# Optimization experiments

Measured on AMD Instinct MI355X. Metric: run time of the kernel, lower is better.

## Reference

```python
import jax, jax.numpy as jnp
import numpy as np

EPS = 1e-6
N_HEAD = 16

def alibi_slopes(n_head):
    # standard ALiBi geometric slopes for power-of-2 head counts
    start = 2.0 ** (-8.0 / n_head)
    return (start ** np.arange(1, n_head + 1)).astype(np.float32)

def rsig(x):
    # rational sigmoid sigma(x) = 0.5 * (x / (|x| + 1) + 1)
    return 0.5 * (x / (jnp.abs(x) + 1.0) + 1.0)

def mr_norm(x, w):
    # RationalMR: x / (mean(|x|) + eps) * weight
    return x / (jnp.mean(jnp.abs(x), axis=-1, keepdims=True) + EPS) * w


def setup_inputs() -> dict:
    key = jax.random.key(0)
    ks = jax.random.split(key, 6)
    d_model, d_ffn = 1024, 4096
    B, T = 1, 2048
    x = jax.random.normal(ks[0], (B, T, d_model), dtype=jnp.float32)
    s = 0.02
    w_qkv = jax.random.normal(ks[1], (3 * d_model, d_model), dtype=jnp.float32) * s
    w_out = jax.random.normal(ks[2], (d_model, d_model), dtype=jnp.float32) * s
    w_merged = jax.random.normal(ks[3], (2 * d_ffn, d_model), dtype=jnp.float32) * s
    w3 = jax.random.normal(ks[4], (d_model, d_ffn), dtype=jnp.float32) * s
    norm1_w = jnp.ones((d_model,), dtype=jnp.float32)
    norm2_w = jnp.ones((d_model,), dtype=jnp.float32)
    return {"x": x, "w_qkv": w_qkv, "w_out": w_out, "w_merged": w_merged,
            "w3": w3, "norm1_w": norm1_w, "norm2_w": norm2_w}


def reference(x, w_qkv, w_out, w_merged, w3, norm1_w, norm2_w):
    B, T, C = x.shape
    H = N_HEAD
    D = C // H
    scale = 1.0 / jnp.sqrt(jnp.float32(D))

    # --- attention sub-block ---
    h = mr_norm(x, norm1_w)
    qkv = (h @ w_qkv.T).reshape(B, T, 3, H, D).transpose(2, 0, 3, 1, 4)  # [3,B,H,T,D]
    q, k, v = qkv[0], qkv[1], qkv[2]
    scores = jnp.einsum('bhtd,bhsd->bhts', q, k) * scale  # [B,H,T,T]
    pos = jnp.arange(T)
    rel = jnp.abs(pos[:, None] - pos[None, :]).astype(jnp.float32)
    slopes = jnp.asarray(alibi_slopes(H))
    scores = scores - rel[None, None] * slopes[None, :, None, None]
    causal = pos[None, :] > pos[:, None]  # mask j > i
    scores = jnp.where(causal[None, None], jnp.float32(-10000.0), scores)
    # rational softmax: sigma(s)^4 / (sum sigma(s)^4 + eps)
    p4 = rsig(scores) ** 4
    probs = p4 / (jnp.sum(p4, axis=-1, keepdims=True) + EPS)
    attn = jnp.einsum('bhts,bhsd->bhtd', probs, v)  # [B,H,T,D]
    attn = attn.transpose(0, 2, 1, 3).reshape(B, T, C)
    x = x + attn @ w_out.T

    # --- FFN sub-block (rational SwiGLU) ---
    h2 = mr_norm(x, norm2_w)
    merged = h2 @ w_merged.T
    gate, val = jnp.split(merged, 2, axis=-1)
    hidden = gate * rsig(gate) * val
    x = x + hidden @ w3.T
    return x
```

## Files before the change

kernel.cpp:

```cpp
#include <hip/hip_runtime.h>
#include <hip/hip_bf16.h>
#include <stdint.h>

typedef unsigned int u32;
typedef unsigned short u16;
typedef __attribute__((ext_vector_type(8))) short bf16x8;
typedef __attribute__((ext_vector_type(4))) float f32x4;

#define MFMA(a, b, c) __builtin_amdgcn_mfma_f32_16x16x32_bf16(a, b, c, 0, 0, 0)

__device__ __forceinline__ u16 f2bf(float f) {
  u32 u = __float_as_uint(f);
  return (u16)((u + 0x7FFFu + ((u >> 16) & 1u)) >> 16);
}
__device__ __forceinline__ float bf2f(u16 h) {
  return __uint_as_float(((u32)h) << 16);
}
__device__ __forceinline__ float rsig_fast(float sc) {
  return 0.5f + 0.5f * sc * __builtin_amdgcn_rcpf(fabsf(sc) + 1.f);
}
__device__ __forceinline__ void async16(void* lds, const void* g) {
  __builtin_amdgcn_global_load_lds((const __attribute__((address_space(1))) u32*)g,
                                   (__attribute__((address_space(3))) u32*)lds, 16, 0, 0);
}

__global__ __launch_bounds__(256) void to_bf16(const float* __restrict__ src,
                                               u16* __restrict__ dst) {
  const size_t i = (size_t)blockIdx.x * 256 + threadIdx.x;
  const float4 a = ((const float4*)src)[2 * i];
  const float4 b = ((const float4*)src)[2 * i + 1];
  ushort4 o0, o1;
  o0.x = f2bf(a.x); o0.y = f2bf(a.y); o0.z = f2bf(a.z); o0.w = f2bf(a.w);
  o1.x = f2bf(b.x); o1.y = f2bf(b.y); o1.z = f2bf(b.z); o1.w = f2bf(b.w);
  ((ushort4*)dst)[2 * i] = o0;
  ((ushort4*)dst)[2 * i + 1] = o1;
}

__global__ __launch_bounds__(256) void mrnorm(const float* __restrict__ x,
                                              const float* __restrict__ wg,
                                              u16* __restrict__ out) {
  const int row = blockIdx.x;
  const int tid = threadIdx.x;
  const float4 v = ((const float4*)(x + (size_t)row * 1024))[tid];
  float s = fabsf(v.x) + fabsf(v.y) + fabsf(v.z) + fabsf(v.w);
#pragma unroll
  for (int off = 1; off < 64; off <<= 1) s += __shfl_xor(s, off);
  __shared__ float red[4];
  if ((tid & 63) == 0) red[tid >> 6] = s;
  __syncthreads();
  const float inv = 1.f / ((red[0] + red[1] + red[2] + red[3]) * (1.f / 1024.f) + 1e-6f);
  const float4 g = ((const float4*)wg)[tid];
  ushort4 o;
  o.x = f2bf(v.x * inv * g.x);
  o.y = f2bf(v.y * inv * g.y);
  o.z = f2bf(v.z * inv * g.z);
  o.w = f2bf(v.w * inv * g.w);
  ((ushort4*)out)[(size_t)row * 256 + tid] = o;
}

template <int EPI, bool DBUF>
__global__ __launch_bounds__(256) void gemm_bt(const u16* __restrict__ A, int lda,
                                               const u16* __restrict__ B, int ldb,
                                               void* __restrict__ C,
                                               const float* __restrict__ resid,
                                               int M, int N, int K) {
  __shared__ __align__(16) u16 As[(DBUF ? 2 : 1) * 128 * 64];
  __shared__ __align__(16) u16 Bs[(DBUF ? 2 : 1) * 128 * 64];
  const int tid = threadIdx.x;
  const int lane = tid & 63;
  const int w = tid >> 6;
  const int wr = (w >> 1) << 6;
  const int wc = (w & 1) << 6;
  const int nbn = N >> 7;
  const int m0 = (blockIdx.x / nbn) << 7;
  const int n0 = (blockIdx.x % nbn) << 7;
  const int l15 = lane & 15;
  const int lhi = lane >> 4;
  A += (size_t)blockIdx.y * K;
  B += (size_t)blockIdx.y * K;

  f32x4 acc[4][4] = {};

  auto stage = [&](int buf, int k0) {
#pragma unroll
    for (int p = 0; p < 4; ++p) {
      const int c = p * 256 + tid;
      const int row = c >> 3;
      const int cb = (c & 7) << 4;
      const int src = cb ^ ((row & 7) << 4);
      async16((char*)As + buf * 16384 + c * 16,
              (const char*)A + ((size_t)(m0 + row) * lda + k0) * 2 + src);
      async16((char*)Bs + buf * 16384 + c * 16,
              (const char*)B + ((size_t)(n0 + row) * ldb + k0) * 2 + src);
    }
  };
  auto compute = [&](int buf) {
#pragma unroll
    for (int kk = 0; kk < 2; ++kk) {
      bf16x8 af[4], bfr[4];
#pragma unroll
      for (int m = 0; m < 4; ++m) {
        const int row = wr + (m << 4) + l15;
        const int off = row * 128 + (((kk << 6) + (lhi << 4)) ^ ((row & 7) << 4));
        af[m] = *(const bf16x8*)((const char*)As + buf * 16384 + off);
      }
#pragma unroll
      for (int n = 0; n < 4; ++n) {
        const int row = wc + (n << 4) + l15;
        const int off = row * 128 + (((kk << 6) + (lhi << 4)) ^ ((row & 7) << 4));
        bfr[n] = *(const bf16x8*)((const char*)Bs + buf * 16384 + off);
      }
#pragma unroll
      for (int m = 0; m < 4; ++m)
#pragma unroll
        for (int n = 0; n < 4; ++n)
          acc[m][n] = MFMA(af[m], bfr[n], acc[m][n]);
    }
  };

  if (DBUF) {
    stage(0, 0);
    __syncthreads();
    int cur = 0;
    for (int k0 = 0; k0 < K; k0 += 64) {
      if (k0 + 64 < K) stage(cur ^ 1, k0 + 64);
      compute(cur);
      __syncthreads();
      cur ^= 1;
    }
  } else {
    for (int k0 = 0; k0 < K; k0 += 64) {
      stage(0, k0);
      __syncthreads();
      compute(0);
      __syncthreads();
    }
  }

  u16* Cp = (u16*)C + (size_t)blockIdx.y * M * N;
#pragma unroll
  for (int m = 0; m < 4; ++m) {
#pragma unroll
    for (int n = 0; n < 4; ++n) {
      const int col = n0 + wc + (n << 4) + l15;
#pragma unroll
      for (int r = 0; r < 4; ++r) {
        const int row = m0 + wr + (m << 4) + (lhi << 2) + r;
        const float v = acc[m][n][r];
        if (EPI == 0) {
          Cp[(size_t)row * N + col] = f2bf(v);
        } else {
          const size_t idx = (size_t)row * N + col;
          ((float*)C)[idx] = resid[idx] + v;
        }
      }
    }
  }
}

__global__ __launch_bounds__(256) void gemm_ffn1(const u16* __restrict__ A,
                                                 const u16* __restrict__ B,
                                                 u16* __restrict__ hid) {
  __shared__ __align__(16) u16 As[2][128 * 64];
  __shared__ __align__(16) u16 Bg[2][64 * 64];
  __shared__ __align__(16) u16 Bv[2][64 * 64];
  const int tid = threadIdx.x;
  const int lane = tid & 63;
  const int w = tid >> 6;
  const int wr = (w >> 1) << 6;
  const int wc = (w & 1) << 5;
  const int m0 = (blockIdx.x >> 6) << 7;
  const int n0 = (blockIdx.x & 63) << 6;
  const int l15 = lane & 15;
  const int lhi = lane >> 4;

  f32x4 ag[4][2] = {};
  f32x4 av[4][2] = {};

  auto stage = [&](int buf, int k0) {
#pragma unroll
    for (int p = 0; p < 4; ++p) {
      const int c = p * 256 + tid;
      const int row = c >> 3;
      const int cb = (c & 7) << 4;
      const int src = cb ^ ((row & 7) << 4);
      async16((char*)As[buf] + c * 16,
              (const char*)A + ((size_t)(m0 + row) * 1024 + k0) * 2 + src);
    }
#pragma unroll
    for (int p = 0; p < 2; ++p) {
      const int c = p * 256 + tid;
      const int row = c >> 3;
      const int cb = (c & 7) << 4;
      const int src = cb ^ ((row & 7) << 4);
      async16((char*)Bg[buf] + c * 16,
              (const char*)B + ((size_t)(n0 + row) * 1024 + k0) * 2 + src);
      async16((char*)Bv[buf] + c * 16,
              (const char*)B + ((size_t)(4096 + n0 + row) * 1024 + k0) * 2 + src);
    }
  };
  auto compute = [&](int buf) {
#pragma unroll
    for (int kk = 0; kk < 2; ++kk) {
      bf16x8 af[4], bgf[2], bvf[2];
#pragma unroll
      for (int m = 0; m < 4; ++m) {
        const int row = wr + (m << 4) + l15;
        const int off = row * 128 + (((kk << 6) + (lhi << 4)) ^ ((row & 7) << 4));
        af[m] = *(const bf16x8*)((const char*)As[buf] + off);
      }
#pragma unroll
      for (int n = 0; n < 2; ++n) {
        const int row = wc + (n << 4) + l15;
        const int off = row * 128 + (((kk << 6) + (lhi << 4)) ^ ((row & 7) << 4));
        bgf[n] = *(const bf16x8*)((const char*)Bg[buf] + off);
        bvf[n] = *(const bf16x8*)((const char*)Bv[buf] + off);
      }
#pragma unroll
      for (int m = 0; m < 4; ++m)
#pragma unroll
        for (int n = 0; n < 2; ++n) {
          ag[m][n] = MFMA(af[m], bgf[n], ag[m][n]);
          av[m][n] = MFMA(af[m], bvf[n], av[m][n]);
        }
    }
  };

  stage(0, 0);
  __syncthreads();
  int cur = 0;
  for (int k0 = 0; k0 < 1024; k0 += 64) {
    if (k0 + 64 < 1024) stage(cur ^ 1, k0 + 64);
    compute(cur);
    __syncthreads();
    cur ^= 1;
  }

#pragma unroll
  for (int m = 0; m < 4; ++m) {
#pragma unroll
    for (int n = 0; n < 2; ++n) {
      const int col = n0 + wc + (n << 4) + l15;
#pragma unroll
      for (int r = 0; r < 4; ++r) {
        const int row = m0 + wr + (m << 4) + (lhi << 2) + r;
        const float g = ag[m][n][r];
        const float v = av[m][n][r];
        hid[(size_t)row * 4096 + col] = f2bf(g * rsig_fast(g) * v);
      }
    }
  }
}

__global__ __launch_bounds__(256) void splitk_reduce(const u16* __restrict__ part,
                                                     const float* __restrict__ resid,
                                                     float* __restrict__ out) {
  const size_t i = ((size_t)blockIdx.x * 256 + threadIdx.x) * 8;
  const float4 r0 = *(const float4*)(resid + i);
  const float4 r1 = *(const float4*)(resid + i + 4);
  float acc[8] = {r0.x, r0.y, r0.z, r0.w, r1.x, r1.y, r1.z, r1.w};
#pragma unroll
  for (int c = 0; c < 4; ++c) {
    const uint4 p = *(const uint4*)(part + (size_t)c * 2097152 + i);
    const u16* ps = (const u16*)&p;
#pragma unroll
    for (int j = 0; j < 8; ++j) acc[j] += bf2f(ps[j]);
  }
  float4 o0 = {acc[0], acc[1], acc[2], acc[3]};
  float4 o1 = {acc[4], acc[5], acc[6], acc[7]};
  *(float4*)(out + i) = o0;
  *(float4*)(out + i + 4) = o1;
}

__global__ __launch_bounds__(256) void transpose_v(const u16* __restrict__ qkv,
                                                   u16* __restrict__ vt) {
  __shared__ __align__(16) u16 tile[64][72];
  const int head = blockIdx.x >> 5;
  const int t0 = (blockIdx.x & 31) << 6;
  const int tid = threadIdx.x;
  const int row = tid >> 2;
  const int cb = (tid & 3) << 4;
  const u16* src = qkv + (size_t)(t0 + row) * 3072 + 2048 + head * 64 + cb;
  *(uint4*)&tile[row][cb] = *(const uint4*)src;
  *(uint4*)&tile[row][cb + 8] = *(const uint4*)(src + 8);
  __syncthreads();
  u16 buf[16];
#pragma unroll
  for (int j = 0; j < 16; ++j) buf[j] = tile[cb + j][row];
  u16* dst = vt + (size_t)(head * 64 + row) * 2048 + t0 + cb;
  *(uint4*)dst = *(const uint4*)&buf[0];
  *(uint4*)(dst + 8) = *(const uint4*)&buf[8];
}

__global__ __launch_bounds__(256) void attn_part(const u16* __restrict__ qkv,
                                                 const u16* __restrict__ vt,
                                                 u16* __restrict__ pnum,
                                                 float* __restrict__ pden) {
  const int id = blockIdx.x;
  const int head = id & 15;
  const int rem = id >> 4;
  int a, g;
  if (rem < 32)      { a = 3; g = rem; }
  else if (rem < 56) { a = 2; g = rem - 32; }
  else if (rem < 72) { a = 1; g = rem - 56; }
  else               { a = 0; g = rem - 72; }
  const int qb = (a << 3) + g / (a + 1);
  const int c = g - (g / (a + 1)) * (a + 1);
  const int slot = head * 80 + ((a * (a + 1)) << 2) + (qb - (a << 3)) * (a + 1) + c;

  __shared__ __align__(16) u16 Ks[2][64 * 64];
  __shared__ __align__(16) u16 Vs[2][64 * 64];
  __shared__ __align__(16) u16 QP[4][16 * 64];
  const int tid = threadIdx.x;
  const int lane = tid & 63;
  const int w = tid >> 6;
  const int l15 = lane & 15;
  const int lhi = lane >> 4;
  const int qbase = qb << 6;
  const float slope = exp2f(-0.5f * (float)(head + 1));

  auto stageKV = [&](int buf, int s0) {
#pragma unroll
    for (int p = 0; p < 2; ++p) {
      const int cc = p * 256 + tid;
      const int row = cc >> 3;
      const int cb = (cc & 7) << 4;
      const int src = cb ^ ((row & 7) << 4);
      async16((char*)Ks[buf] + cc * 16,
              (const char*)qkv + ((size_t)(s0 + row) * 3072 + 1024 + head * 64) * 2 + src);
      async16((char*)Vs[buf] + cc * 16,
              (const char*)vt + ((size_t)(head * 64 + row) * 2048 + s0) * 2 + src);
    }
  };

  const int sfirst = c << 9;
  const int smax = min(qbase, sfirst + 448);
#pragma unroll
  for (int p = 0; p < 2; ++p) {
    const int cc = p * 256 + tid;
    const int row = cc >> 3;
    const int cb = (cc & 7) << 4;
    const int src = cb ^ ((row & 7) << 4);
    async16((char*)QP + cc * 16,
            (const char*)qkv + ((size_t)(qbase + row) * 3072 + head * 64) * 2 + src);
  }
  stageKV(0, sfirst);
  __syncthreads();

  bf16x8 qf[2];
#pragma unroll
  for (int kk = 0; kk < 2; ++kk) {
    const int row = (w << 4) + l15;
    const int off = row * 128 + (((kk << 6) + (lhi << 4)) ^ ((row & 7) << 4));
    qf[kk] = *(const bf16x8*)((const char*)QP + off);
  }

  f32x4 oacc[4] = {};
  float rs[4] = {0.f, 0.f, 0.f, 0.f};
  u16* pw = (u16*)QP[w];
  int cur = 0;

  for (int s0 = sfirst; s0 <= smax; s0 += 64) {
    if (s0 + 64 <= smax) stageKV(cur ^ 1, s0 + 64);
    const char* Kc = (const char*)Ks[cur];
    const char* Vc = (const char*)Vs[cur];

    bf16x8 kf[4][2];
#pragma unroll
    for (int bb = 0; bb < 4; ++bb)
#pragma unroll
      for (int kk = 0; kk < 2; ++kk) {
        const int row = (bb << 4) + l15;
        const int off = row * 128 + (((kk << 6) + (lhi << 4)) ^ ((row & 7) << 4));
        kf[bb][kk] = *(const bf16x8*)(Kc + off);
      }
    f32x4 sa[4];
#pragma unroll
    for (int bb = 0; bb < 4; ++bb) {
      f32x4 z = {0.f, 0.f, 0.f, 0.f};
      z = MFMA(qf[0], kf[bb][0], z);
      sa[bb] = MFMA(qf[1], kf[bb][1], z);
    }
#pragma unroll
    for (int bb = 0; bb < 4; ++bb) {
      const int s_abs = s0 + (bb << 4) + l15;
#pragma unroll
      for (int r = 0; r < 4; ++r) {
        const int prow = (lhi << 2) + r;
        const int q_abs = qbase + (w << 4) + prow;
        float p4 = 0.f;
        if (s_abs <= q_abs) {
          const float sc = sa[bb][r] * 0.125f - slope * (float)(q_abs - s_abs);
          const float t = rsig_fast(sc);
          const float t2 = t * t;
          p4 = t2 * t2;
        }
        rs[r] += p4;
        const int pcol2 = ((bb << 4) + l15) << 1;
        const int poff = prow * 128 + (pcol2 ^ ((prow & 7) << 4));
        *(u16*)((char*)pw + poff) = f2bf(p4);
      }
    }
    bf16x8 pf[2];
#pragma unroll
    for (int kk = 0; kk < 2; ++kk) {
      const int row = l15;
      const int off = row * 128 + (((kk << 6) + (lhi << 4)) ^ ((row & 7) << 4));
      pf[kk] = *(const bf16x8*)((const char*)pw + off);
    }
#pragma unroll
    for (int db = 0; db < 4; ++db) {
#pragma unroll
      for (int kk = 0; kk < 2; ++kk) {
        const int row = (db << 4) + l15;
        const int off = row * 128 + (((kk << 6) + (lhi << 4)) ^ ((row & 7) << 4));
        const bf16x8 vf = *(const bf16x8*)(Vc + off);
        oacc[db] = MFMA(pf[kk], vf, oacc[db]);
      }
    }
    __syncthreads();
    cur ^= 1;
  }

#pragma unroll
  for (int r = 0; r < 4; ++r) {
    float v = rs[r];
    v += __shfl_xor(v, 1);
    v += __shfl_xor(v, 2);
    v += __shfl_xor(v, 4);
    v += __shfl_xor(v, 8);
    rs[r] = v;
  }
  if (l15 == 0) {
#pragma unroll
    for (int r = 0; r < 4; ++r)
      pden[(size_t)slot * 64 + (w << 4) + (lhi << 2) + r] = rs[r];
  }
  __syncthreads();
#pragma unroll
  for (int db = 0; db < 4; ++db)
#pragma unroll
    for (int r = 0; r < 4; ++r)
      pw[((lhi << 2) + r) * 64 + (db << 4) + l15] = f2bf(oacc[db][r]);
  __syncthreads();
  {
    const int row = lane >> 2;
    const int cb = (lane & 3) << 4;
    const u16* s = pw + row * 64 + cb;
    const uint4 d0 = *(const uint4*)s;
    const uint4 d1 = *(const uint4*)(s + 8);
    u16* dst = pnum + (size_t)slot * 4096 + ((w << 4) + row) * 64 + cb;
    *(uint4*)dst = d0;
    *(uint4*)(dst + 8) = d1;
  }
}

__global__ __launch_bounds__(256) void attn_merge(const u16* __restrict__ pnum,
                                                  const float* __restrict__ pden,
                                                  u16* __restrict__ out) {
  const int head = blockIdx.x >> 5;
  const int qb = blockIdx.x & 31;
  const int nc = (qb >> 3) + 1;
  const int a = qb >> 3, b = qb & 7;
  const int slot0 = head * 80 + ((a * (a + 1)) << 2) + b * (a + 1);
  const int tid = threadIdx.x;
  const int row = tid >> 2;
  const int c0 = (tid & 3) << 4;

  float acc[16] = {};
  float den = 0.f;
  for (int ci = 0; ci < nc; ++ci) {
    const int slot = slot0 + ci;
    den += pden[(size_t)slot * 64 + row];
    const u16* np = pnum + (size_t)slot * 4096 + row * 64 + c0;
    const uint4 n0 = *(const uint4*)np;
    const uint4 n1 = *(const uint4*)(np + 8);
    const u16* ns0 = (const u16*)&n0;
    const u16* ns1 = (const u16*)&n1;
#pragma unroll
    for (int j = 0; j < 8; ++j) {
      acc[j] += bf2f(ns0[j]);
      acc[8 + j] += bf2f(ns1[j]);
    }
  }
  const float inv = 1.f / (den + 1e-6f);
  u16 ob[16];
#pragma unroll
  for (int j = 0; j < 16; ++j) ob[j] = f2bf(acc[j] * inv);
  u16* dst = out + (size_t)((qb << 6) + row) * 1024 + head * 64 + c0;
  *(uint4*)dst = *(const uint4*)&ob[0];
  *(uint4*)(dst + 8) = *(const uint4*)&ob[8];
}

extern "C" void kernel_launch(void* const* d_in, const int* in_sizes, int n_in,
                              void* d_out, int out_size, void* d_ws, size_t ws_size,
                              hipStream_t stream) {
  const float* x     = (const float*)d_in[0];
  const float* wqkv  = (const float*)d_in[1];
  const float* wout  = (const float*)d_in[2];
  const float* wmer  = (const float*)d_in[3];
  const float* w3    = (const float*)d_in[4];
  const float* n1w   = (const float*)d_in[5];
  const float* n2w   = (const float*)d_in[6];
  char* ws = (char*)d_ws;

  u16*   WQKV = (u16*)(ws + 0);
  u16*   WOUT = (u16*)(ws + 6291456);
  u16*   WMER = (u16*)(ws + 8388608);
  u16*   W3B  = (u16*)(ws + 25165824);
  float* X1   = (float*)(ws + 33554432);
  u16*   QKV  = (u16*)(ws + 41943040);
  u16*   VT   = (u16*)(ws + 54525952);
  u16*   ATTN = (u16*)(ws + 58720256);
  u16*   PNUM = (u16*)(ws + 62914560);
  float* PDEN = (float*)(ws + 73400320);
  u16*   HID  = (u16*)(ws + 41943040);
  u16*   PART = (u16*)(ws + 8388608);
  u16*   H    = (u16*)(ws + 75497472);
  u16*   H2   = (u16*)(ws + 75497472);

  to_bf16<<<1536, 256, 0, stream>>>(wqkv, WQKV);
  to_bf16<<<512, 256, 0, stream>>>(wout, WOUT);
  to_bf16<<<4096, 256, 0, stream>>>(wmer, WMER);
  to_bf16<<<2048, 256, 0, stream>>>(w3, W3B);

  mrnorm<<<2048, 256, 0, stream>>>(x, n1w, H);
  gemm_bt<0, true><<<16 * 24, 256, 0, stream>>>(H, 1024, WQKV, 1024, QKV, nullptr,
                                                2048, 3072, 1024);
  transpose_v<<<512, 256, 0, stream>>>(QKV, VT);
  attn_part<<<1280, 256, 0, stream>>>(QKV, VT, PNUM, PDEN);
  attn_merge<<<512, 256, 0, stream>>>(PNUM, PDEN, ATTN);
  gemm_bt<1, true><<<16 * 8, 256, 0, stream>>>(ATTN, 1024, WOUT, 1024, X1, x,
                                               2048, 1024, 1024);

  mrnorm<<<2048, 256, 0, stream>>>(X1, n2w, H2);
  gemm_ffn1<<<1024, 256, 0, stream>>>(H2, WMER, HID);
  gemm_bt<0, true><<<dim3(16 * 8, 4), 256, 0, stream>>>(HID, 4096, W3B, 4096, PART,
                                                        nullptr, 2048, 1024, 1024);
  splitk_reduce<<<1024, 256, 0, stream>>>(PART, X1, (float*)d_out);
}
```

Baseline: 180.3 us.

## Merge weight conversions into one launch and load attention K/V directly from global

The four fp32-to-bf16 weight conversion launches are merged into a single launch that picks its source and destination by block index, removing per-launch overhead. Separately, the attention kernel drops its double-buffered LDS staging of Q, K and V and reads the MFMA fragments straight from global memory, removing the per-tile barrier and LDS traffic. In exchange, each wave now issues its own uncoalesced-ish global loads with no prefetch overlap and no sharing across the four waves, so K/V reads rely on cache hits.

```diff
diff --git a/kernel.cpp b/kernel.cpp
--- a/kernel.cpp
+++ b/kernel.cpp
@@ -24,14 +24,22 @@
                                    (__attribute__((address_space(3))) u32*)lds, 16, 0, 0);
 }
 
-__global__ __launch_bounds__(256) void to_bf16(const float* __restrict__ src,
-                                               u16* __restrict__ dst) {
-  const size_t i = (size_t)blockIdx.x * 256 + threadIdx.x;
+__global__ __launch_bounds__(256) void to_bf16_all(const float* __restrict__ s0, u16* __restrict__ d0,
+                                                   const float* __restrict__ s1, u16* __restrict__ d1,
+                                                   const float* __restrict__ s2, u16* __restrict__ d2,
+                                                   const float* __restrict__ s3, u16* __restrict__ d3) {
+  int b = blockIdx.x;
+  const float* src; u16* dst;
+  if (b < 1536)      { src = s0; dst = d0; }
+  else if (b < 2048) { src = s1; dst = d1; b -= 1536; }
+  else if (b < 6144) { src = s2; dst = d2; b -= 2048; }
+  else               { src = s3; dst = d3; b -= 6144; }
+  const size_t i = (size_t)b * 256 + threadIdx.x;
   const float4 a = ((const float4*)src)[2 * i];
-  const float4 b = ((const float4*)src)[2 * i + 1];
+  const float4 c = ((const float4*)src)[2 * i + 1];
   ushort4 o0, o1;
   o0.x = f2bf(a.x); o0.y = f2bf(a.y); o0.z = f2bf(a.z); o0.w = f2bf(a.w);
-  o1.x = f2bf(b.x); o1.y = f2bf(b.y); o1.z = f2bf(b.z); o1.w = f2bf(b.w);
+  o1.x = f2bf(c.x); o1.y = f2bf(c.y); o1.z = f2bf(c.z); o1.w = f2bf(c.w);
   ((ushort4*)dst)[2 * i] = o0;
   ((ushort4*)dst)[2 * i + 1] = o1;
 }
@@ -308,8 +316,6 @@
   const int c = g - (g / (a + 1)) * (a + 1);
   const int slot = head * 80 + ((a * (a + 1)) << 2) + (qb - (a << 3)) * (a + 1) + c;
 
-  __shared__ __align__(16) u16 Ks[2][64 * 64];
-  __shared__ __align__(16) u16 Vs[2][64 * 64];
   __shared__ __align__(16) u16 QP[4][16 * 64];
   const int tid = threadIdx.x;
   const int lane = tid & 63;
@@ -319,61 +325,26 @@
   const int qbase = qb << 6;
   const float slope = exp2f(-0.5f * (float)(head + 1));
 
-  auto stageKV = [&](int buf, int s0) {
-#pragma unroll
-    for (int p = 0; p < 2; ++p) {
-      const int cc = p * 256 + tid;
-      const int row = cc >> 3;
-      const int cb = (cc & 7) << 4;
-      const int src = cb ^ ((row & 7) << 4);
-      async16((char*)Ks[buf] + cc * 16,
-              (const char*)qkv + ((size_t)(s0 + row) * 3072 + 1024 + head * 64) * 2 + src);
-      async16((char*)Vs[buf] + cc * 16,
-              (const char*)vt + ((size_t)(head * 64 + row) * 2048 + s0) * 2 + src);
-    }
-  };
-
-  const int sfirst = c << 9;
-  const int smax = min(qbase, sfirst + 448);
-#pragma unroll
-  for (int p = 0; p < 2; ++p) {
-    const int cc = p * 256 + tid;
-    const int row = cc >> 3;
-    const int cb = (cc & 7) << 4;
-    const int src = cb ^ ((row & 7) << 4);
-    async16((char*)QP + cc * 16,
-            (const char*)qkv + ((size_t)(qbase + row) * 3072 + head * 64) * 2 + src);
-  }
-  stageKV(0, sfirst);
-  __syncthreads();
-
   bf16x8 qf[2];
 #pragma unroll
-  for (int kk = 0; kk < 2; ++kk) {
-    const int row = (w << 4) + l15;
-    const int off = row * 128 + (((kk << 6) + (lhi << 4)) ^ ((row & 7) << 4));
-    qf[kk] = *(const bf16x8*)((const char*)QP + off);
-  }
+  for (int kk = 0; kk < 2; ++kk)
+    qf[kk] = *(const bf16x8*)(qkv + (size_t)(qbase + (w << 4) + l15) * 3072 +
+                              head * 64 + (kk << 5) + (lhi << 3));
 
   f32x4 oacc[4] = {};
   float rs[4] = {0.f, 0.f, 0.f, 0.f};
   u16* pw = (u16*)QP[w];
-  int cur = 0;
+  const int sfirst = c << 9;
+  const int smax = min(qbase, sfirst + 448);
 
   for (int s0 = sfirst; s0 <= smax; s0 += 64) {
-    if (s0 + 64 <= smax) stageKV(cur ^ 1, s0 + 64);
-    const char* Kc = (const char*)Ks[cur];
-    const char* Vc = (const char*)Vs[cur];
-
     bf16x8 kf[4][2];
 #pragma unroll
     for (int bb = 0; bb < 4; ++bb)
 #pragma unroll
-      for (int kk = 0; kk < 2; ++kk) {
-        const int row = (bb << 4) + l15;
-        const int off = row * 128 + (((kk << 6) + (lhi << 4)) ^ ((row & 7) << 4));
-        kf[bb][kk] = *(const bf16x8*)(Kc + off);
-      }
+      for (int kk = 0; kk < 2; ++kk)
+        kf[bb][kk] = *(const bf16x8*)(qkv + (size_t)(s0 + (bb << 4) + l15) * 3072 +
+                                      1024 + head * 64 + (kk << 5) + (lhi << 3));
     f32x4 sa[4];
 #pragma unroll
     for (int bb = 0; bb < 4; ++bb) {
@@ -404,22 +375,18 @@
     bf16x8 pf[2];
 #pragma unroll
     for (int kk = 0; kk < 2; ++kk) {
-      const int row = l15;
-      const int off = row * 128 + (((kk << 6) + (lhi << 4)) ^ ((row & 7) << 4));
+      const int off = l15 * 128 + (((kk << 6) + (lhi << 4)) ^ ((l15 & 7) << 4));
       pf[kk] = *(const bf16x8*)((const char*)pw + off);
     }
 #pragma unroll
     for (int db = 0; db < 4; ++db) {
 #pragma unroll
       for (int kk = 0; kk < 2; ++kk) {
-        const int row = (db << 4) + l15;
-        const int off = row * 128 + (((kk << 6) + (lhi << 4)) ^ ((row & 7) << 4));
-        const bf16x8 vf = *(const bf16x8*)(Vc + off);
+        const bf16x8 vf = *(const bf16x8*)(vt +
+            (size_t)(head * 64 + (db << 4) + l15) * 2048 + s0 + (kk << 5) + (lhi << 3));
         oacc[db] = MFMA(pf[kk], vf, oacc[db]);
       }
     }
-    __syncthreads();
-    cur ^= 1;
   }
 
 #pragma unroll
@@ -519,10 +486,7 @@
   u16*   H    = (u16*)(ws + 75497472);
   u16*   H2   = (u16*)(ws + 75497472);
 
-  to_bf16<<<1536, 256, 0, stream>>>(wqkv, WQKV);
-  to_bf16<<<512, 256, 0, stream>>>(wout, WOUT);
-  to_bf16<<<4096, 256, 0, stream>>>(wmer, WMER);
-  to_bf16<<<2048, 256, 0, stream>>>(w3, W3B);
+  to_bf16_all<<<8192, 256, 0, stream>>>(wqkv, WQKV, wout, WOUT, wmer, WMER, w3, W3B);
 
   mrnorm<<<2048, 256, 0, stream>>>(x, n1w, H);
   gemm_bt<0, true><<<16 * 24, 256, 0, stream>>>(H, 1024, WQKV, 1024, QKV, nullptr,
```

Measured after the change: 221.0 us. 1.23x slower.
